# Performance work log

Measured on AMD Instinct MI355X. Metric: run time of the kernel, lower is better.

## Reference

```python
import jax, jax.numpy as jnp
import numpy as np

N_NODES = 50000
N_EDGES = 800000
DIMX = 64
DIMY = 32
NSMAT = 64
N_MID = 6  # six hidden nsmat->nsmat layers between the input and output projections


def setup_inputs() -> dict:
    key = jax.random.key(0)
    ks = jax.random.split(key, 10)
    node_features = jax.random.normal(ks[0], (N_NODES, DIMX), dtype=jnp.float32)
    edge_index = jax.random.randint(ks[1], (2, N_EDGES), 0, N_NODES, dtype=jnp.int64)
    s_in = 1.0 / np.sqrt(DIMX)
    s_mid = 1.0 / np.sqrt(NSMAT)
    w_in = jax.random.uniform(ks[2], (DIMX, NSMAT), jnp.float32, -s_in, s_in)
    b_in = jax.random.uniform(ks[3], (NSMAT,), jnp.float32, -s_in, s_in)
    w_mid = jax.random.uniform(ks[4], (N_MID, NSMAT, NSMAT), jnp.float32, -s_mid, s_mid)
    b_mid = jax.random.uniform(ks[5], (N_MID, NSMAT), jnp.float32, -s_mid, s_mid)
    w_out = jax.random.uniform(ks[6], (NSMAT, DIMY * DIMX), jnp.float32, -s_mid, s_mid)
    b_out = jax.random.uniform(ks[7], (DIMY * DIMX,), jnp.float32, -s_mid, s_mid)
    return {"node_features": node_features, "edge_index": edge_index,
            "w_in": w_in, "b_in": b_in, "w_mid": w_mid, "b_mid": b_mid,
            "w_out": w_out, "b_out": b_out}


def reference(node_features, edge_index, w_in, b_in, w_mid, b_mid, w_out, b_out):
    # per-node MLP producing a [dimy, dimx] sheaf matrix
    h = jax.nn.relu(node_features @ w_in + b_in)
    for i in range(N_MID):  # fixed small layer count
        h = jax.nn.relu(h @ w_mid[i] + b_mid[i])
    smat = (h @ w_out + b_out).reshape(-1, DIMY, DIMX)  # [N, dimy, dimx]
    # batched matrix-vector transform: q_n = smat_n @ x_n
    q = jnp.einsum('nyx,nx->ny', smat, node_features)  # [N, dimy]
    # LightGCN conv: out_i = sum_{(j->i) in E} q_j / sqrt(deg_j * deg_i)
    row, col = edge_index[0], edge_index[1]
    deg = jax.ops.segment_sum(jnp.ones((N_EDGES,), q.dtype), col, num_segments=N_NODES)
    dinv = jnp.where(deg > 0, jax.lax.rsqrt(jnp.maximum(deg, 1.0)), 0.0)
    norm = dinv[row] * dinv[col]  # [E]
    out = jax.ops.segment_sum(norm[:, None] * q[row], col, num_segments=N_NODES)
    return out
```

## Files before the change

kernel.cpp:

```cpp
#include <hip/hip_runtime.h>
#include <cstddef>

#define N_NODES_C 50000
#define N_NODES_PAD 50048
#define N_EDGES_C 800000
#define CAP 64

typedef _Float16 f16x8 __attribute__((ext_vector_type(8)));
typedef float    f32x4 __attribute__((ext_vector_type(4)));

constexpr int XSTR = 72;
constexpr int MQ_BLOCKS   = 782;
constexpr int FILL_BLOCKS = 782;
constexpr int DEG_BLOCKS  = 782;

__device__ __forceinline__ void gll16(const void* g, void* l) {
    __builtin_amdgcn_global_load_lds(
        (const __attribute__((address_space(1))) void*)g,
        (__attribute__((address_space(3))) void*)l, 16, 0, 0);
}

__global__ void prep_deg_kernel(const float* __restrict__ w_in,
                                const float* __restrict__ w_mid,
                                const float* __restrict__ w_out,
                                const int* __restrict__ col,
                                _Float16* __restrict__ wT,
                                _Float16* __restrict__ W3T,
                                int* __restrict__ deg,
                                unsigned char* __restrict__ rank8)
{
    const int b = blockIdx.x;
    if (b < 624) {
        const int idx = b * 256 + threadIdx.x;
        if (idx < 7 * 4096) {
            const int l = idx >> 12, rem = idx & 4095;
            const int k = rem >> 6, j = rem & 63;
            const float v = (l == 0) ? w_in[k * 64 + j]
                                     : w_mid[(size_t)(l - 1) * 4096 + k * 64 + j];
            wT[(size_t)l * 4096 + j * 64 + k] = (_Float16)v;
        } else {
            const int i2 = idx - 7 * 4096;
            const int k = i2 >> 11, r = i2 & 2047;
            const int c = k >> 3;
            const int pos = ((c ^ (r & 7)) << 3) | (k & 7);
            W3T[(size_t)r * 64 + pos] = (_Float16)w_out[(size_t)k * 2048 + r];
        }
    } else {
        const int e0 = (b - 624) * 1024 + threadIdx.x;
        #pragma unroll
        for (int k = 0; k < 4; ++k) {
            const int e = e0 + k * 256;
            if (e < N_EDGES_C)
                rank8[e] = (unsigned char)atomicAdd(&deg[col[e]], 1);
        }
    }
}

__launch_bounds__(256, 4)
__global__ void mega_kernel(const float* __restrict__ xf,
                            const float* __restrict__ b_in,
                            const float* __restrict__ b_mid,
                            const _Float16* __restrict__ wT,
                            const _Float16* __restrict__ W3T,
                            const float* __restrict__ b_out,
                            const int* __restrict__ deg,
                            float* __restrict__ qs,
                            const int* __restrict__ row,
                            const int* __restrict__ col,
                            const unsigned char* __restrict__ rank8,
                            unsigned short* __restrict__ src16)
{
    __shared__ _Float16 smem[16896];

    if (blockIdx.x >= MQ_BLOCKS) {
        const int base = (blockIdx.x - MQ_BLOCKS) * 1024 + threadIdx.x;
        #pragma unroll
        for (int u = 0; u < 4; ++u) {
            const int e = base + u * 256;
            if (e < N_EDGES_C) {
                const int c = col[e];
                const int r = rank8[e];
                src16[(size_t)c * CAP + r] = (unsigned short)row[e];
            }
        }
        return;
    }

    const int t    = threadIdx.x;
    const int w    = t >> 6;
    const int lane = t & 63;
    const int quad = lane >> 4;
    const int lrow = lane & 15;
    const int node0 = blockIdx.x * 64 + w * 16;
    _Float16* hb = &smem[w * 16 * XSTR];

    {
        const int n = min(node0 + lrow, N_NODES_C - 1);
        const float4* src4 = (const float4*)(xf + (size_t)n * 64 + quad * 16);
        _Float16 tmp[16];
        #pragma unroll
        for (int i = 0; i < 4; ++i) {
            const float4 v = src4[i];
            tmp[i * 4 + 0] = (_Float16)v.x;
            tmp[i * 4 + 1] = (_Float16)v.y;
            tmp[i * 4 + 2] = (_Float16)v.z;
            tmp[i * 4 + 3] = (_Float16)v.w;
        }
        *(f16x8*)&hb[lrow * XSTR + quad * 16]     = *(f16x8*)&tmp[0];
        *(f16x8*)&hb[lrow * XSTR + quad * 16 + 8] = *(f16x8*)&tmp[8];
    }

    {
        const _Float16* wTl = wT;
        const float* bsrc = b_in;
        for (int l = 0; l < 7; ++l) {
            const f16x8 A0 = *(const f16x8*)&hb[lrow * XSTR + quad * 8];
            const f16x8 A1 = *(const f16x8*)&hb[lrow * XSTR + 32 + quad * 8];
            #pragma unroll
            for (int Nt = 0; Nt < 4; ++Nt) {
                const f16x8 B0 = *(const f16x8*)(wTl + (Nt * 16 + lrow) * 64 + quad * 8);
                const f16x8 B1 = *(const f16x8*)(wTl + (Nt * 16 + lrow) * 64 + 32 + quad * 8);
                const float bias = bsrc[Nt * 16 + lrow];
                f32x4 C = {0.f, 0.f, 0.f, 0.f};
                C = __builtin_amdgcn_mfma_f32_16x16x32_f16(A0, B0, C, 0, 0, 0);
                C = __builtin_amdgcn_mfma_f32_16x16x32_f16(A1, B1, C, 0, 0, 0);
                #pragma unroll
                for (int r = 0; r < 4; ++r) {
                    const float v = fmaxf(C[r] + bias, 0.f);
                    hb[(quad * 4 + r) * XSTR + Nt * 16 + lrow] = (_Float16)v;
                }
            }
            wTl += 4096;
            bsrc = b_mid + (size_t)l * 64;
        }
    }

    const int ra = node0 + lrow;
    const int na = min(ra, N_NODES_C - 1);

    f16x8 Bha[2];
    #pragma unroll
    for (int ks = 0; ks < 2; ++ks)
        Bha[ks] = *(const f16x8*)&hb[lrow * XSTR + ks * 32 + quad * 8];
    float4 xca[4];
    #pragma unroll
    for (int xt = 0; xt < 4; ++xt)
        xca[xt] = *(const float4*)(xf + (size_t)na * 64 + xt * 16 + quad * 4);
    const int dg = deg[na];
    const float dva = (dg > 0) ? rsqrtf((float)dg) : 0.f;

    __syncthreads();

    {
        float* lb = (float*)smem;
        const float* gb = b_out + (size_t)(w * 64 + lane) * 4;
        gll16(gb,        lb + w * 256);
        gll16(gb + 1024, lb + 1024 + w * 256);
        #pragma unroll
        for (int s = 0; s < 2; ++s) {
            _Float16* ld = &smem[4608 + s * 4096 + w * 512];
            const _Float16* gs = W3T + (size_t)s * 4096 + (size_t)(w * 64 + lane) * 8;
            gll16(gs,        ld);
            gll16(gs + 2048, ld + 2048);
        }
    }

    const int swz = lrow & 7;
    const int cp0 = ((quad)     ^ swz) * 8;
    const int cp1 = ((4 + quad) ^ swz) * 8;
    const float* lbf = (const float*)smem;

    int rcur = 0;
    for (int y = 0; y < 32; ++y) {
        if (y == 0)      asm volatile("s_waitcnt vmcnt(2)" ::: "memory");
        else if (y == 1) asm volatile("s_waitcnt vmcnt(3)" ::: "memory");
        else             asm volatile("s_waitcnt vmcnt(4)" ::: "memory");
        __builtin_amdgcn_s_barrier();
        __builtin_amdgcn_sched_barrier(0);

        {
            const int ys = (y + 2) & 31;
            const int ri = (rcur == 0) ? 2 : rcur - 1;
            _Float16* ld = &smem[4608 + ri * 4096 + w * 512];
            const _Float16* gs = W3T + (size_t)ys * 4096 + (size_t)(w * 64 + lane) * 8;
            gll16(gs,        ld);
            gll16(gs + 2048, ld + 2048);
        }

        const _Float16* cur = &smem[4608 + rcur * 4096];
        float qa = 0.f;
        #pragma unroll
        for (int xt = 0; xt < 4; ++xt) {
            const _Float16* rp = cur + (xt * 16 + lrow) * 64;
            const f16x8 A0 = *(const f16x8*)(rp + cp0);
            const f16x8 A1 = *(const f16x8*)(rp + cp1);
            f32x4 Ca = {0.f, 0.f, 0.f, 0.f};
            Ca = __builtin_amdgcn_mfma_f32_16x16x32_f16(A0, Bha[0], Ca, 0, 0, 0);
            Ca = __builtin_amdgcn_mfma_f32_16x16x32_f16(A1, Bha[1], Ca, 0, 0, 0);

            const float4 bf = *(const float4*)(lbf + y * 64 + xt * 16 + quad * 4);
            qa += (Ca[0] + bf.x) * xca[xt].x + (Ca[1] + bf.y) * xca[xt].y
                + (Ca[2] + bf.z) * xca[xt].z + (Ca[3] + bf.w) * xca[xt].w;
        }
        qa += __shfl_xor(qa, 16);
        qa += __shfl_xor(qa, 32);

        if (quad == (y >> 3)) {
            qs[(size_t)ra * 32 + y] = qa * dva;
        }

        rcur = (rcur == 2) ? 0 : rcur + 1;
    }
}

__global__ void gather_kernel(const int* __restrict__ deg,
                              const unsigned short* __restrict__ src16,
                              const float* __restrict__ qs,
                              float* __restrict__ out)
{
    const int t = threadIdx.x;
    const int node = blockIdx.x * 32 + (t >> 3);
    if (node >= N_NODES_C) return;
    const int yq = (t & 7) * 4;
    const int d = deg[node];
    const unsigned short* sp = src16 + (size_t)node * CAP;
    float4 acc = {0.f, 0.f, 0.f, 0.f};
    int s = 0;
    for (; s + 4 <= d; s += 4) {
        const ushort4 r4 = *(const ushort4*)(sp + s);
        const float4 a0 = *(const float4*)(qs + (size_t)r4.x * 32 + yq);
        const float4 a1 = *(const float4*)(qs + (size_t)r4.y * 32 + yq);
        const float4 a2 = *(const float4*)(qs + (size_t)r4.z * 32 + yq);
        const float4 a3 = *(const float4*)(qs + (size_t)r4.w * 32 + yq);
        acc.x += a0.x + a1.x + a2.x + a3.x;
        acc.y += a0.y + a1.y + a2.y + a3.y;
        acc.z += a0.z + a1.z + a2.z + a3.z;
        acc.w += a0.w + a1.w + a2.w + a3.w;
    }
    for (; s < d; ++s) {
        const float4 a = *(const float4*)(qs + (size_t)sp[s] * 32 + yq);
        acc.x += a.x; acc.y += a.y; acc.z += a.z; acc.w += a.w;
    }
    const float dv = (d > 0) ? rsqrtf((float)d) : 0.f;
    float4 r;
    r.x = acc.x * dv; r.y = acc.y * dv; r.z = acc.z * dv; r.w = acc.w * dv;
    *(float4*)(out + (size_t)node * 32 + yq) = r;
}

extern "C" void kernel_launch(void* const* d_in, const int* in_sizes, int n_in,
                              void* d_out, int out_size, void* d_ws, size_t ws_size,
                              hipStream_t stream)
{
    const float* xf    = (const float*)d_in[0];
    const int*   eidx  = (const int*)d_in[1];
    const float* w_in  = (const float*)d_in[2];
    const float* b_in  = (const float*)d_in[3];
    const float* w_mid = (const float*)d_in[4];
    const float* b_mid = (const float*)d_in[5];
    const float* w_out = (const float*)d_in[6];
    const float* b_out = (const float*)d_in[7];
    float* out = (float*)d_out;

    const int* row = eidx;
    const int* col = eidx + N_EDGES_C;

    char* ws = (char*)d_ws;
    float*          qs    = (float*)(ws + 0);
    int*            deg   = (int*)(ws + 6406144);
    _Float16*       wT    = (_Float16*)(ws + 6606336);
    _Float16*       W3T   = (_Float16*)(ws + 6663680);
    unsigned char*  rank8 = (unsigned char*)(ws + 6925824);
    unsigned short* src16 = (unsigned short*)(ws + 7725824);

    hipMemsetAsync(deg, 0, 50048 * sizeof(int), stream);

    prep_deg_kernel<<<dim3(624 + DEG_BLOCKS), dim3(256), 0, stream>>>(
        w_in, w_mid, w_out, col, wT, W3T, deg, rank8);

    mega_kernel<<<dim3(MQ_BLOCKS + FILL_BLOCKS), dim3(256), 0, stream>>>(
        xf, b_in, b_mid, wT, W3T, b_out, deg, qs, row, col, rank8, src16);

    gather_kernel<<<dim3(1563), dim3(256), 0, stream>>>(deg, src16, qs, out);
}
```

Baseline: 188.7 us.

## Move degree counting into mega kernel and scale q in separate fill pass

Degree atomics now run alongside the MLP blocks inside mega_kernel, and the weight-prep kernel shrinks to weight conversion only. The degree normalisation of q moves out of the MLP kernel into a new fill_scale kernel, which also builds the src16 adjacency lists. The aim is to overlap the atomic degree pass with the MLP compute and shorten the critical path of the prep launch. The cost is an extra read-modify-write pass over qs (about 6.4 MB).

```diff
diff --git a/kernel.cpp b/kernel.cpp
--- a/kernel.cpp
+++ b/kernel.cpp
@@ -11,8 +11,9 @@
 
 constexpr int XSTR = 72;
 constexpr int MQ_BLOCKS   = 782;
+constexpr int DEG_BLOCKS  = 782;
 constexpr int FILL_BLOCKS = 782;
-constexpr int DEG_BLOCKS  = 782;
+constexpr int SCALE_BLOCKS = 391;
 
 __device__ __forceinline__ void gll16(const void* g, void* l) {
     __builtin_amdgcn_global_load_lds(
@@ -20,39 +21,25 @@
         (__attribute__((address_space(3))) void*)l, 16, 0, 0);
 }
 
-__global__ void prep_deg_kernel(const float* __restrict__ w_in,
-                                const float* __restrict__ w_mid,
-                                const float* __restrict__ w_out,
-                                const int* __restrict__ col,
-                                _Float16* __restrict__ wT,
-                                _Float16* __restrict__ W3T,
-                                int* __restrict__ deg,
-                                unsigned char* __restrict__ rank8)
-{
-    const int b = blockIdx.x;
-    if (b < 624) {
-        const int idx = b * 256 + threadIdx.x;
-        if (idx < 7 * 4096) {
-            const int l = idx >> 12, rem = idx & 4095;
-            const int k = rem >> 6, j = rem & 63;
-            const float v = (l == 0) ? w_in[k * 64 + j]
-                                     : w_mid[(size_t)(l - 1) * 4096 + k * 64 + j];
-            wT[(size_t)l * 4096 + j * 64 + k] = (_Float16)v;
-        } else {
-            const int i2 = idx - 7 * 4096;
-            const int k = i2 >> 11, r = i2 & 2047;
-            const int c = k >> 3;
-            const int pos = ((c ^ (r & 7)) << 3) | (k & 7);
-            W3T[(size_t)r * 64 + pos] = (_Float16)w_out[(size_t)k * 2048 + r];
-        }
+__global__ void prep_w_kernel(const float* __restrict__ w_in,
+                              const float* __restrict__ w_mid,
+                              const float* __restrict__ w_out,
+                              _Float16* __restrict__ wT,
+                              _Float16* __restrict__ W3T)
+{
+    const int idx = blockIdx.x * 256 + threadIdx.x;
+    if (idx < 7 * 4096) {
+        const int l = idx >> 12, rem = idx & 4095;
+        const int k = rem >> 6, j = rem & 63;
+        const float v = (l == 0) ? w_in[k * 64 + j]
+                                 : w_mid[(size_t)(l - 1) * 4096 + k * 64 + j];
+        wT[(size_t)l * 4096 + j * 64 + k] = (_Float16)v;
     } else {
-        const int e0 = (b - 624) * 1024 + threadIdx.x;
-        #pragma unroll
-        for (int k = 0; k < 4; ++k) {
-            const int e = e0 + k * 256;
-            if (e < N_EDGES_C)
-                rank8[e] = (unsigned char)atomicAdd(&deg[col[e]], 1);
-        }
+        const int i2 = idx - 7 * 4096;
+        const int k = i2 >> 11, r = i2 & 2047;
+        const int c = k >> 3;
+        const int pos = ((c ^ (r & 7)) << 3) | (k & 7);
+        W3T[(size_t)r * 64 + pos] = (_Float16)w_out[(size_t)k * 2048 + r];
     }
 }
 
@@ -63,12 +50,10 @@
                             const _Float16* __restrict__ wT,
                             const _Float16* __restrict__ W3T,
                             const float* __restrict__ b_out,
-                            const int* __restrict__ deg,
                             float* __restrict__ qs,
-                            const int* __restrict__ row,
                             const int* __restrict__ col,
-                            const unsigned char* __restrict__ rank8,
-                            unsigned short* __restrict__ src16)
+                            int* __restrict__ deg,
+                            unsigned char* __restrict__ rank8)
 {
     __shared__ _Float16 smem[16896];
 
@@ -77,11 +62,8 @@
         #pragma unroll
         for (int u = 0; u < 4; ++u) {
             const int e = base + u * 256;
-            if (e < N_EDGES_C) {
-                const int c = col[e];
-                const int r = rank8[e];
-                src16[(size_t)c * CAP + r] = (unsigned short)row[e];
-            }
+            if (e < N_EDGES_C)
+                rank8[e] = (unsigned char)atomicAdd(&deg[col[e]], 1);
         }
         return;
     }
@@ -146,8 +128,6 @@
     #pragma unroll
     for (int xt = 0; xt < 4; ++xt)
         xca[xt] = *(const float4*)(xf + (size_t)na * 64 + xt * 16 + quad * 4);
-    const int dg = deg[na];
-    const float dva = (dg > 0) ? rsqrtf((float)dg) : 0.f;
 
     __syncthreads();
 
@@ -206,10 +186,44 @@
         qa += __shfl_xor(qa, 32);
 
         if (quad == (y >> 3)) {
-            qs[(size_t)ra * 32 + y] = qa * dva;
+            qs[(size_t)ra * 32 + y] = qa;
         }
 
         rcur = (rcur == 2) ? 0 : rcur + 1;
+    }
+}
+
+__global__ void fill_scale_kernel(const int* __restrict__ row,
+                                  const int* __restrict__ col,
+                                  const unsigned char* __restrict__ rank8,
+                                  const int* __restrict__ deg,
+                                  float* __restrict__ qs,
+                                  unsigned short* __restrict__ src16)
+{
+    if (blockIdx.x < FILL_BLOCKS) {
+        const int base = blockIdx.x * 1024 + threadIdx.x;
+        #pragma unroll
+        for (int u = 0; u < 4; ++u) {
+            const int e = base + u * 256;
+            if (e < N_EDGES_C) {
+                const int c = col[e];
+                const int r = rank8[e];
+                src16[(size_t)c * CAP + r] = (unsigned short)row[e];
+            }
+        }
+    } else {
+        const int sb = blockIdx.x - FILL_BLOCKS;
+        #pragma unroll
+        for (int k = 0; k < 4; ++k) {
+            const int idx4 = k * (SCALE_BLOCKS * 256) + sb * 256 + threadIdx.x;
+            const int rown = idx4 >> 3;
+            const int d = (rown < N_NODES_C) ? deg[rown] : 0;
+            const float dv = (d > 0) ? rsqrtf((float)d) : 0.f;
+            float4* p = (float4*)qs + idx4;
+            float4 v = *p;
+            v.x *= dv; v.y *= dv; v.z *= dv; v.w *= dv;
+            *p = v;
+        }
     }
 }
 
@@ -274,11 +288,13 @@
 
     hipMemsetAsync(deg, 0, 50048 * sizeof(int), stream);
 
-    prep_deg_kernel<<<dim3(624 + DEG_BLOCKS), dim3(256), 0, stream>>>(
-        w_in, w_mid, w_out, col, wT, W3T, deg, rank8);
-
-    mega_kernel<<<dim3(MQ_BLOCKS + FILL_BLOCKS), dim3(256), 0, stream>>>(
-        xf, b_in, b_mid, wT, W3T, b_out, deg, qs, row, col, rank8, src16);
+    prep_w_kernel<<<dim3(624), dim3(256), 0, stream>>>(w_in, w_mid, w_out, wT, W3T);
+
+    mega_kernel<<<dim3(MQ_BLOCKS + DEG_BLOCKS), dim3(256), 0, stream>>>(
+        xf, b_in, b_mid, wT, W3T, b_out, qs, col, deg, rank8);
+
+    fill_scale_kernel<<<dim3(FILL_BLOCKS + SCALE_BLOCKS), dim3(256), 0, stream>>>(
+        row, col, rank8, deg, qs, src16);
 
     gather_kernel<<<dim3(1563), dim3(256), 0, stream>>>(deg, src16, qs, out);
 }
```

Result: faster. 168.2 us (-10.9%).
